# Optimization experiments

Measured on AMD Instinct MI355X. Metric: run time of the kernel, lower is better.

## Reference

```python
import jax, jax.numpy as jnp
import numpy as np

EPS = 1e-12

def setup_inputs() -> dict:
    key = jax.random.key(0)
    k1, k2 = jax.random.split(key)
    N, L, C = 32768, 256, 64
    mu = jax.random.uniform(k1, (N, L), dtype=jnp.float32)
    leaf_scores = jax.random.normal(k2, (L, C), dtype=jnp.float32)
    return {"mu": mu, "leaf_scores": leaf_scores}

def reference(mu, leaf_scores):
    # log path probabilities, clamped for numerical safety: (N, L)
    log_mu = jnp.log(jnp.clip(mu, EPS, None))
    # per-leaf class log-probs: (L, C)
    logQ = jax.nn.log_softmax(leaf_scores, axis=1)
    # y[n,k] = logsumexp_l( log_mu[n,l] + logQ[l,k] )  -> (N, C)
    scores = log_mu[:, :, None] + logQ[None, :, :]  # (N, L, C)
    return jax.scipy.special.logsumexp(scores, axis=1)
```

## Files before the change

kernel.cpp:

```cpp
#include <hip/hip_runtime.h>
#include <math.h>

#define NN 32768
#define LL 256
#define CC 64
#define EPSV 1e-12f

typedef __attribute__((ext_vector_type(8))) _Float16 half8;
typedef __attribute__((ext_vector_type(4))) float f32x4;

__global__ __launch_bounds__(64) void prep_kernel(
    const float* __restrict__ scores, _Float16* __restrict__ wsB) {
    const int l = blockIdx.x;
    const int k = threadIdx.x;
    float v = scores[(size_t)l * CC + k];
    float mx = v;
    #pragma unroll
    for (int off = 32; off > 0; off >>= 1) mx = fmaxf(mx, __shfl_xor(mx, off));
    float e = expf(v - mx);
    float sum = e;
    #pragma unroll
    for (int off = 32; off > 0; off >>= 1) sum += __shfl_xor(sum, off);
    _Float16 h = (_Float16)(e / sum);

    const int s = l >> 5;
    const int w = l & 31;
    const int q = w >> 3;
    const int j = w & 7;
    const int t = k >> 4;
    const int m = k & 15;
    wsB[((s * 4 + t) * 64 + q * 16 + m) * 8 + j] = h;
}

__global__ __launch_bounds__(256) void leaf_mix_mfma_kernel(
    const float* __restrict__ mu, const float4* __restrict__ wsB,
    float* __restrict__ out) {
    __shared__ float Bs[8192];

    const int tid = threadIdx.x;
    const int wid = tid >> 6;
    const int lane = tid & 63;
    const int quad = lane >> 4;
    const int m = lane & 15;

    const size_t row = (size_t)blockIdx.x * 64 + wid * 16 + m;
    const float* arow = mu + row * LL + quad * 8;
    float4 a[16];
    #pragma unroll
    for (int s = 0; s < 8; ++s) {
        a[2 * s]     = *(const float4*)(arow + s * 32);
        a[2 * s + 1] = *(const float4*)(arow + s * 32 + 4);
    }

    {
        float4* dst = (float4*)Bs;
        #pragma unroll
        for (int i = 0; i < 8; ++i) dst[tid + 256 * i] = wsB[tid + 256 * i];
    }
    __syncthreads();

    f32x4 acc[4] = {{0.f, 0.f, 0.f, 0.f}, {0.f, 0.f, 0.f, 0.f},
                    {0.f, 0.f, 0.f, 0.f}, {0.f, 0.f, 0.f, 0.f}};

    #pragma unroll
    for (int s = 0; s < 8; ++s) {
        const float f[8] = {a[2 * s].x, a[2 * s].y, a[2 * s].z, a[2 * s].w,
                            a[2 * s + 1].x, a[2 * s + 1].y, a[2 * s + 1].z, a[2 * s + 1].w};
        half8 ahi, alo;
        #pragma unroll
        for (int e = 0; e < 8; ++e) {
            const float x = fmaxf(f[e], EPSV);
            const _Float16 h = (_Float16)x;
            ahi[e] = h;
            alo[e] = (_Float16)(x - (float)h);
        }
        #pragma unroll
        for (int t = 0; t < 4; ++t) {
            const half8 b = ((const half8*)(Bs + (s * 4 + t) * 256))[lane];
            acc[t] = __builtin_amdgcn_mfma_f32_16x16x32_f16(ahi, b, acc[t], 0, 0, 0);
            acc[t] = __builtin_amdgcn_mfma_f32_16x16x32_f16(alo, b, acc[t], 0, 0, 0);
        }
    }

    const size_t outRow0 = (size_t)blockIdx.x * 64 + wid * 16 + quad * 4;
    #pragma unroll
    for (int t = 0; t < 4; ++t)
        #pragma unroll
        for (int r = 0; r < 4; ++r)
            out[(outRow0 + r) * CC + t * 16 + m] = logf(acc[t][r]);
}

extern "C" void kernel_launch(void* const* d_in, const int* in_sizes, int n_in,
                              void* d_out, int out_size, void* d_ws, size_t ws_size,
                              hipStream_t stream) {
    const float* mu     = (const float*)d_in[0];
    const float* scores = (const float*)d_in[1];
    float* out = (float*)d_out;

    prep_kernel<<<LL, CC, 0, stream>>>(scores, (_Float16*)d_ws);
    leaf_mix_mfma_kernel<<<NN / 64, 256, 0, stream>>>(mu, (const float4*)d_ws, out);
}
```

Before: 79.52 us.

## Fuse softmax prep into main kernel and drop hi/lo split MFMA

Removes the separate prep kernel launch: every block now loads the raw leaf scores, computes the row softmax in shared memory, and packs the fp16 B fragments itself. The mu operand is now a single fp16 conversion instead of a hi/lo split, which halves the MFMA count. The cost is redundant softmax work in all 512 blocks and more shared memory per block. Dropping the low half also lowers precision of the mixing sum.

```diff
diff --git a/kernel.cpp b/kernel.cpp
--- a/kernel.cpp
+++ b/kernel.cpp
@@ -5,43 +5,29 @@
 #define LL 256
 #define CC 64
 #define EPSV 1e-12f
+#define SP 65
 
 typedef __attribute__((ext_vector_type(8))) _Float16 half8;
 typedef __attribute__((ext_vector_type(4))) float f32x4;
 
-__global__ __launch_bounds__(64) void prep_kernel(
-    const float* __restrict__ scores, _Float16* __restrict__ wsB) {
-    const int l = blockIdx.x;
-    const int k = threadIdx.x;
-    float v = scores[(size_t)l * CC + k];
-    float mx = v;
-    #pragma unroll
-    for (int off = 32; off > 0; off >>= 1) mx = fmaxf(mx, __shfl_xor(mx, off));
-    float e = expf(v - mx);
-    float sum = e;
-    #pragma unroll
-    for (int off = 32; off > 0; off >>= 1) sum += __shfl_xor(sum, off);
-    _Float16 h = (_Float16)(e / sum);
-
-    const int s = l >> 5;
-    const int w = l & 31;
-    const int q = w >> 3;
-    const int j = w & 7;
-    const int t = k >> 4;
-    const int m = k & 15;
-    wsB[((s * 4 + t) * 64 + q * 16 + m) * 8 + j] = h;
-}
-
-__global__ __launch_bounds__(256) void leaf_mix_mfma_kernel(
-    const float* __restrict__ mu, const float4* __restrict__ wsB,
+__global__ __launch_bounds__(256, 2) void fused_leaf_mix_kernel(
+    const float* __restrict__ mu, const float* __restrict__ scores,
     float* __restrict__ out) {
-    __shared__ float Bs[8192];
+    __shared__ __align__(16) unsigned char smem[256 * SP * 4 + 256 * 4];
+    float* S = (float*)smem;
+    float* rinv = (float*)(smem + 256 * SP * 4);
+    half8* F = (half8*)smem;
 
     const int tid = threadIdx.x;
     const int wid = tid >> 6;
     const int lane = tid & 63;
     const int quad = lane >> 4;
     const int m = lane & 15;
+
+    const float4* s4 = (const float4*)scores;
+    float4 sv[16];
+    #pragma unroll
+    for (int i = 0; i < 16; ++i) sv[i] = s4[tid + 256 * i];
 
     const size_t row = (size_t)blockIdx.x * 64 + wid * 16 + m;
     const float* arow = mu + row * LL + quad * 8;
@@ -52,33 +38,64 @@
         a[2 * s + 1] = *(const float4*)(arow + s * 32 + 4);
     }
 
+    #pragma unroll
+    for (int i = 0; i < 16; ++i) {
+        const int f = tid + 256 * i;
+        const int r = f >> 4;
+        const int c4 = f & 15;
+        S[r * SP + c4 * 4 + 0] = sv[i].x;
+        S[r * SP + c4 * 4 + 1] = sv[i].y;
+        S[r * SP + c4 * 4 + 2] = sv[i].z;
+        S[r * SP + c4 * 4 + 3] = sv[i].w;
+    }
+    __syncthreads();
+
     {
-        float4* dst = (float4*)Bs;
+        float rv[64];
         #pragma unroll
-        for (int i = 0; i < 8; ++i) dst[tid + 256 * i] = wsB[tid + 256 * i];
+        for (int c = 0; c < 64; ++c) rv[c] = S[tid * SP + c];
+        float mx = rv[0];
+        #pragma unroll
+        for (int c = 1; c < 64; ++c) mx = fmaxf(mx, rv[c]);
+        float sum = 0.f;
+        #pragma unroll
+        for (int c = 0; c < 64; ++c) { rv[c] = expf(rv[c] - mx); sum += rv[c]; }
+        #pragma unroll
+        for (int c = 0; c < 64; ++c) S[tid * SP + c] = rv[c];
+        rinv[tid] = 1.0f / sum;
     }
+    __syncthreads();
+
+    half8 breg[8];
+    #pragma unroll
+    for (int i = 0; i < 8; ++i) {
+        const int g = wid * 8 + i;
+        const int s = g >> 2, tn = g & 3;
+        #pragma unroll
+        for (int j = 0; j < 8; ++j) {
+            const int k = s * 32 + quad * 8 + j;
+            breg[i][j] = (_Float16)(S[k * SP + tn * 16 + m] * rinv[k]);
+        }
+    }
+    __syncthreads();
+
+    #pragma unroll
+    for (int i = 0; i < 8; ++i) F[(wid * 8 + i) * 64 + lane] = breg[i];
     __syncthreads();
 
     f32x4 acc[4] = {{0.f, 0.f, 0.f, 0.f}, {0.f, 0.f, 0.f, 0.f},
                     {0.f, 0.f, 0.f, 0.f}, {0.f, 0.f, 0.f, 0.f}};
-
     #pragma unroll
     for (int s = 0; s < 8; ++s) {
-        const float f[8] = {a[2 * s].x, a[2 * s].y, a[2 * s].z, a[2 * s].w,
-                            a[2 * s + 1].x, a[2 * s + 1].y, a[2 * s + 1].z, a[2 * s + 1].w};
-        half8 ahi, alo;
+        const float f8[8] = {a[2 * s].x, a[2 * s].y, a[2 * s].z, a[2 * s].w,
+                             a[2 * s + 1].x, a[2 * s + 1].y, a[2 * s + 1].z, a[2 * s + 1].w};
+        half8 ah;
         #pragma unroll
-        for (int e = 0; e < 8; ++e) {
-            const float x = fmaxf(f[e], EPSV);
-            const _Float16 h = (_Float16)x;
-            ahi[e] = h;
-            alo[e] = (_Float16)(x - (float)h);
-        }
+        for (int e = 0; e < 8; ++e) ah[e] = (_Float16)fmaxf(f8[e], EPSV);
         #pragma unroll
         for (int t = 0; t < 4; ++t) {
-            const half8 b = ((const half8*)(Bs + (s * 4 + t) * 256))[lane];
-            acc[t] = __builtin_amdgcn_mfma_f32_16x16x32_f16(ahi, b, acc[t], 0, 0, 0);
-            acc[t] = __builtin_amdgcn_mfma_f32_16x16x32_f16(alo, b, acc[t], 0, 0, 0);
+            const half8 b = F[(s * 4 + t) * 64 + lane];
+            acc[t] = __builtin_amdgcn_mfma_f32_16x16x32_f16(ah, b, acc[t], 0, 0, 0);
         }
     }
 
@@ -96,7 +113,7 @@
     const float* mu     = (const float*)d_in[0];
     const float* scores = (const float*)d_in[1];
     float* out = (float*)d_out;
+    (void)d_ws; (void)ws_size;
 
-    prep_kernel<<<LL, CC, 0, stream>>>(scores, (_Float16*)d_ws);
-    leaf_mix_mfma_kernel<<<NN / 64, 256, 0, stream>>>(mu, (const float4*)d_ws, out);
+    fused_leaf_mix_kernel<<<NN / 64, 256, 0, stream>>>(mu, scores, out);
 }
```

Result: slower. 82.32 us (+3.5%).
